# Kernel optimization log

Hardware: AMD Instinct MI355X
Metric: run time of the kernel (lower is better)

Reference implementation:

```python
import jax, jax.numpy as jnp
import numpy as np

B, S, D = 8, 4096, 768
HEADS = 12
NEIGHBORS = 2
DILATION = 1
KERNEL = 1 + 2 * NEIGHBORS  # 5
DIM_HEAD = D // HEADS


def setup_inputs() -> dict:
    key = jax.random.key(0)
    ks = jax.random.split(key, 11)
    sc = 1.0 / np.sqrt(D)
    return {
        "x": jax.random.normal(ks[0], (B, S, D), dtype=jnp.float32),
        "Wq": jax.random.normal(ks[1], (D, D), dtype=jnp.float32) * sc,
        "bq": jax.random.normal(ks[2], (D,), dtype=jnp.float32) * 0.02,
        "Wk": jax.random.normal(ks[3], (D, D), dtype=jnp.float32) * sc,
        "bk": jax.random.normal(ks[4], (D,), dtype=jnp.float32) * 0.02,
        "Wv": jax.random.normal(ks[5], (D, D), dtype=jnp.float32) * sc,
        "bv": jax.random.normal(ks[6], (D,), dtype=jnp.float32) * 0.02,
        "Wo": jax.random.normal(ks[7], (D, D), dtype=jnp.float32) * sc,
        "bo": jax.random.normal(ks[8], (D,), dtype=jnp.float32) * 0.02,
        "gamma": jnp.ones((D,), dtype=jnp.float32),
        "beta": jnp.zeros((D,), dtype=jnp.float32),
    }


def _extract_seq_patches(x, kernel_size, dilation):
    # [B, S, D] -> [B, S, kernel_size, D] of dilated local windows, zero-padded.
    seq_len = x.shape[1]
    patch_size = kernel_size + (dilation - 1) * (kernel_size - 1)
    pad_r = (patch_size - 1) // 2
    pad_l = patch_size - pad_r - 1
    xp = jnp.pad(x, ((0, 0), (pad_l, pad_r), (0, 0)))
    # small fixed loop over kernel positions (kernel_size = 5)
    return jnp.stack([xp[:, i:i + seq_len] for i in range(0, patch_size, dilation)], axis=2)


def reference(x, Wq, bq, Wk, bk, Wv, bv, Wo, bo, gamma, beta):
    patches = _extract_seq_patches(x, KERNEL, DILATION)  # [B, S, K, D]
    q = x @ Wq + bq                                       # [B, S, D]
    k = patches @ Wk + bk                                 # [B, S, K, D]
    v = patches @ Wv + bv                                 # [B, S, K, D]
    # split heads
    q = q.reshape(B, S, HEADS, DIM_HEAD)
    k = k.reshape(B, S, KERNEL, HEADS, DIM_HEAD)
    v = v.reshape(B, S, KERNEL, HEADS, DIM_HEAD)
    scale = jnp.sqrt(jnp.asarray(DIM_HEAD, dtype=q.dtype))
    scores = jnp.einsum('bshd,bskhd->bshk', q, k) / scale  # [B, S, H, K]
    p = jax.nn.softmax(scores, axis=-1)
    att = jnp.einsum('bshk,bskhd->bshd', p, v)             # [B, S, H, dh]
    att = att.reshape(B, S, D)
    att = att @ Wo + bo
    y = att + x
    # LayerNorm over last dim
    mu = jnp.mean(y, axis=-1, keepdims=True)
    var = jnp.var(y, axis=-1, keepdims=True)
    y = (y - mu) / jnp.sqrt(var + 1e-5) * gamma + beta
    return y
```

## Files before the change

kernel.cpp:

```cpp
#include <hip/hip_runtime.h>

#define B_  8
#define S_  4096
#define D_  768
#define H_  12
#define M_  (B_ * S_)
#define NQKV_ 2304
#define NTILES 12

typedef unsigned short u16;
typedef __attribute__((ext_vector_type(4))) float  f32x4;
typedef __attribute__((ext_vector_type(8))) __bf16 bf16x8;
typedef __attribute__((ext_vector_type(4))) u16    u16x4;

#define GAS __attribute__((address_space(1)))
#define LAS __attribute__((address_space(3)))

__device__ __forceinline__ u16 f2bf(float f) {
    unsigned u = __float_as_uint(f);
    u += 0x7FFF + ((u >> 16) & 1);
    return (u16)(u >> 16);
}
__device__ __forceinline__ float bf2f(u16 h) {
    return __uint_as_float(((unsigned)h) << 16);
}

__device__ __forceinline__ void gload_lds16(const void* g, void* l) {
    __builtin_amdgcn_global_load_lds((const GAS void*)g, (LAS void*)l, 16, 0, 0);
}

__device__ __forceinline__ int xcd_swz(int bid, int nwg) {
    return (bid & 7) * (nwg >> 3) + (bid >> 3);
}

__global__ __launch_bounds__(256) void castx_kernel(const float* __restrict__ x,
                                                    u16* __restrict__ xb) {
    const int i = blockIdx.x * 256 + threadIdx.x;
    const float4 v = ((const float4*)x)[i];
    u16x4 o;
    o.x = f2bf(v.x); o.y = f2bf(v.y); o.z = f2bf(v.z); o.w = f2bf(v.w);
    ((u16x4*)xb)[i] = o;
}

__global__ __launch_bounds__(256) void wtrans_kernel(const float* __restrict__ Wq,
                                                     const float* __restrict__ Wk,
                                                     const float* __restrict__ Wv,
                                                     const float* __restrict__ Wo,
                                                     u16* __restrict__ Wb) {
    const float* W = (blockIdx.z == 0) ? Wq : (blockIdx.z == 1) ? Wk
                   : (blockIdx.z == 2) ? Wv : Wo;
    u16* O = Wb + (size_t)blockIdx.z * D_ * D_;
    __shared__ float tile[32][33];
    const int tx = threadIdx.x & 31, ty = threadIdx.x >> 5;
    const int k0 = blockIdx.y * 32, n0 = blockIdx.x * 32;
#pragma unroll
    for (int j = 0; j < 4; j++)
        tile[ty + j * 8][tx] = W[(size_t)(k0 + ty + j * 8) * D_ + n0 + tx];
    __syncthreads();
#pragma unroll
    for (int j = 0; j < 4; j++)
        O[(size_t)(n0 + ty + j * 8) * D_ + k0 + tx] = f2bf(tile[tx][ty + j * 8]);
}


#define SYNC_NOVM()                                          \
    __builtin_amdgcn_sched_barrier(0);                       \
    __builtin_amdgcn_s_barrier();                            \
    asm volatile("s_waitcnt lgkmcnt(0)" ::: "memory");       \
    __builtin_amdgcn_sched_barrier(0)

#define SYNC_VM(N)                                           \
    __builtin_amdgcn_sched_barrier(0);                       \
    asm volatile("s_waitcnt vmcnt(" #N ")" ::: "memory");    \
    __builtin_amdgcn_s_barrier();                            \
    asm volatile("s_waitcnt lgkmcnt(0)" ::: "memory");       \
    __builtin_amdgcn_sched_barrier(0)

#define TRAIL()                                              \
    __builtin_amdgcn_sched_barrier(0);                       \
    __builtin_amdgcn_s_barrier()

#define MFMA_Q(AF, BF, MO, NO)                                               \
    __builtin_amdgcn_s_setprio(1);                                           \
    _Pragma("unroll") for (int mi = 0; mi < 4; ++mi)                         \
        _Pragma("unroll") for (int ni = 0; ni < 2; ++ni)                     \
            _Pragma("unroll") for (int kh = 0; kh < 2; ++kh)                 \
                acc[mi + MO][ni + NO] =                                      \
                    __builtin_amdgcn_mfma_f32_16x16x32_bf16(                 \
                        AF[mi][kh], BF[ni][kh], acc[mi + MO][ni + NO], 0, 0, 0); \
    __builtin_amdgcn_s_setprio(0)

template <int MODE>
__global__ __launch_bounds__(512, 2) void gemm8_kernel(
    const u16* __restrict__ A, const u16* __restrict__ Wb,
    const float* __restrict__ b0, const float* __restrict__ b1,
    const float* __restrict__ b2,
    u16* __restrict__ outb, const u16* __restrict__ xres) {
    extern __shared__ char lds[];

    const int t = threadIdx.x;
    const int w = t >> 6, l = t & 63;
    const int wm = w >> 2, wn = w & 3;

    const int NTN = (MODE == 0) ? 9 : 3;
    const int work = xcd_swz(blockIdx.x, gridDim.x);
    const int mt = work / NTN, nt = work % NTN;
    const int m0 = mt * 256;
    const int n0 = nt * 256;
    const int widx = (MODE == 0) ? (n0 / D_) : 3;
    const int n0w = n0 - ((MODE == 0) ? widx * D_ : 0);

    const int srow   = t >> 3;
    const int schunk = (t & 7) ^ (srow & 7);
    const u16* Asrc = A + (size_t)(m0 + srow) * D_ + schunk * 8;
    const u16* Bsrc = Wb + (size_t)widx * (D_ * D_) + (size_t)(n0w + srow) * D_ + schunk * 8;

    auto STAGE_A = [&](int h, int tk, int db) {
        const u16* s = Asrc + (size_t)(h * 128) * D_ + tk * 64;
        char* d = lds + db * 65536 + h * 16384 + (w << 10);
        gload_lds16(s, d);
        gload_lds16(s + 64 * D_, d + 8192);
    };
    auto STAGE_B = [&](int h, int tk, int db) {
        const u16* s = Bsrc + (size_t)(h * 128) * D_ + tk * 64;
        char* d = lds + db * 65536 + 32768 + h * 16384 + (w << 10);
        gload_lds16(s, d);
        gload_lds16(s + 64 * D_, d + 8192);
    };

    const int ck0 = (((l >> 4) ^ (l & 7)) << 4);
    const int ck1 = ((((l >> 4) + 4) ^ (l & 7)) << 4);
    const int aRowB = (wm * 128 + (l & 15)) * 128;
    const int bRowB = 32768 + (wn * 64 + (l & 15)) * 128;
#define LDSREAD(off) (*(const bf16x8*)(lds + (off)))

    f32x4 acc[8][4];
#pragma unroll
    for (int i = 0; i < 8; i++)
#pragma unroll
        for (int j = 0; j < 4; j++) acc[i][j] = (f32x4){0.f, 0.f, 0.f, 0.f};

    bf16x8 Alo[4][2], Ahi[4][2], Ba[2][2], Bb[2][2];

    STAGE_A(0, 0, 0); STAGE_A(1, 0, 0); STAGE_B(0, 0, 0); STAGE_B(1, 0, 0);
    STAGE_A(0, 1, 1); STAGE_A(1, 1, 1); STAGE_B(0, 1, 1);
    __builtin_amdgcn_sched_barrier(0);
    asm volatile("s_waitcnt vmcnt(6)" ::: "memory");
    __builtin_amdgcn_s_barrier();
#pragma unroll
    for (int mi = 0; mi < 4; ++mi) {
        Alo[mi][0] = LDSREAD(aRowB + mi * 2048 + ck0);
        Alo[mi][1] = LDSREAD(aRowB + mi * 2048 + ck1);
    }
#pragma unroll
    for (int ni = 0; ni < 2; ++ni) {
        Ba[ni][0] = LDSREAD(bRowB + ni * 2048 + ck0);
        Ba[ni][1] = LDSREAD(bRowB + ni * 2048 + ck1);
    }

    for (int X = 0; X < NTILES; ++X) {
        const int bX = X & 1;
        const int L0off = bX << 16;
        const int L1off = (bX ^ 1) << 16;
        int t1 = X + 1; if (t1 >= NTILES) t1 -= NTILES;
        int t2 = X + 2; if (t2 >= NTILES) t2 -= NTILES;

#pragma unroll
        for (int mi = 0; mi < 4; ++mi) {
            Ahi[mi][0] = LDSREAD(L0off + aRowB + (mi + 4) * 2048 + ck0);
            Ahi[mi][1] = LDSREAD(L0off + aRowB + (mi + 4) * 2048 + ck1);
        }
#pragma unroll
        for (int ni = 0; ni < 2; ++ni) {
            Bb[ni][0] = LDSREAD(L0off + bRowB + (ni + 2) * 2048 + ck0);
            Bb[ni][1] = LDSREAD(L0off + bRowB + (ni + 2) * 2048 + ck1);
        }
        STAGE_B(1, t1, bX ^ 1);
        SYNC_NOVM();
        MFMA_Q(Alo, Ba, 0, 0);
        TRAIL();

        STAGE_A(0, t2, bX);
        SYNC_VM(6);
        MFMA_Q(Alo, Bb, 0, 2);
        TRAIL();

#pragma unroll
        for (int mi = 0; mi < 4; ++mi) {
            Alo[mi][0] = LDSREAD(L1off + aRowB + mi * 2048 + ck0);
            Alo[mi][1] = LDSREAD(L1off + aRowB + mi * 2048 + ck1);
        }
        STAGE_A(1, t2, bX);
        SYNC_VM(4);
        MFMA_Q(Ahi, Ba, 4, 0);
        TRAIL();

#pragma unroll
        for (int ni = 0; ni < 2; ++ni) {
            Ba[ni][0] = LDSREAD(L1off + bRowB + ni * 2048 + ck0);
            Ba[ni][1] = LDSREAD(L1off + bRowB + ni * 2048 + ck1);
        }
        STAGE_B(0, t2, bX);
        SYNC_VM(6);
        MFMA_Q(Ahi, Bb, 4, 2);
        TRAIL();
    }

    const int crow0 = m0 + wm * 128 + ((l >> 4) << 2);
    const int ccol0 = n0 + wn * 64 + (l & 15);
    if (MODE == 0) {
        const float* bias = (widx == 0) ? b0 : (widx == 1) ? b1 : b2;
        const int bcol0 = ccol0 - widx * D_;
#pragma unroll
        for (int mi = 0; mi < 8; ++mi)
#pragma unroll
            for (int ni = 0; ni < 4; ++ni) {
                const float bv = bias[bcol0 + ni * 16];
#pragma unroll
                for (int r = 0; r < 4; ++r)
                    outb[(size_t)(crow0 + mi * 16 + r) * NQKV_ + ccol0 + ni * 16] =
                        f2bf(acc[mi][ni][r] + bv);
            }
    } else {
#pragma unroll
        for (int mi = 0; mi < 8; ++mi)
#pragma unroll
            for (int ni = 0; ni < 4; ++ni) {
                const int col = ccol0 + ni * 16;
                const float bv = b0[col];
#pragma unroll
                for (int r = 0; r < 4; ++r) {
                    const size_t idx = (size_t)(crow0 + mi * 16 + r) * D_ + col;
                    outb[idx] = f2bf(acc[mi][ni][r] + bv + bf2f(xres[idx]));
                }
            }
    }
}

__global__ __launch_bounds__(256) void attn_kernel(const u16* __restrict__ QKV,
                                                   const float* __restrict__ bk,
                                                   const float* __restrict__ bv,
                                                   u16* __restrict__ att) {
    const int gw = xcd_swz(blockIdx.x, gridDim.x) * 4 + (threadIdx.x >> 6);
    const int l  = threadIdx.x & 63;
    const int hq = gw % 3;
    const int m  = gw / 3;
    const int s  = m & (S_ - 1);
    const int col = hq * 256 + l * 4;
    const u16* base = QKV + (size_t)m * NQKV_;

    const u16x4 qv = *(const u16x4*)(base + col);
    float qf[4];
#pragma unroll
    for (int j = 0; j < 4; j++) qf[j] = bf2f(qv[j]);

    float sc[5];
#pragma unroll
    for (int i = 0; i < 5; i++) {
        const int sp = s + i - 2;
        float p;
        if (sp >= 0 && sp < S_) {
            const u16x4 kv = *(const u16x4*)(base + (i - 2) * NQKV_ + D_ + col);
            p = qf[0] * bf2f(kv[0]) + qf[1] * bf2f(kv[1])
              + qf[2] * bf2f(kv[2]) + qf[3] * bf2f(kv[3]);
        } else {
            const float4 kb = *(const float4*)(bk + col);
            p = qf[0] * kb.x + qf[1] * kb.y + qf[2] * kb.z + qf[3] * kb.w;
        }
#pragma unroll
        for (int off = 1; off < 16; off <<= 1) p += __shfl_xor(p, off, 64);
        sc[i] = p * 0.125f;
    }
    float mx = sc[0];
#pragma unroll
    for (int i = 1; i < 5; i++) mx = fmaxf(mx, sc[i]);
    float e[5], sum = 0.f;
#pragma unroll
    for (int i = 0; i < 5; i++) { e[i] = __expf(sc[i] - mx); sum += e[i]; }
    const float inv = 1.f / sum;

    float o[4] = {0.f, 0.f, 0.f, 0.f};
#pragma unroll
    for (int i = 0; i < 5; i++) {
        const float wgt = e[i] * inv;
        const int sp = s + i - 2;
        if (sp >= 0 && sp < S_) {
            const u16x4 vv = *(const u16x4*)(base + (i - 2) * NQKV_ + 2 * D_ + col);
#pragma unroll
            for (int j = 0; j < 4; j++) o[j] += wgt * bf2f(vv[j]);
        } else {
            const float4 vb = *(const float4*)(bv + col);
            o[0] += wgt * vb.x; o[1] += wgt * vb.y;
            o[2] += wgt * vb.z; o[3] += wgt * vb.w;
        }
    }
    u16x4 ov;
#pragma unroll
    for (int j = 0; j < 4; j++) ov[j] = f2bf(o[j]);
    *(u16x4*)(att + (size_t)m * D_ + col) = ov;
}

__global__ __launch_bounds__(256) void ln_kernel(const u16* __restrict__ Yb,
                                                 const float* __restrict__ gamma,
                                                 const float* __restrict__ beta,
                                                 float* __restrict__ out) {
    const int row = blockIdx.x;
    const u16* r = Yb + (size_t)row * D_;
    const int t = threadIdx.x;
    const float v0 = bf2f(r[t]), v1 = bf2f(r[t + 256]), v2 = bf2f(r[t + 512]);
    float s  = v0 + v1 + v2;
    float s2 = v0 * v0 + v1 * v1 + v2 * v2;
#pragma unroll
    for (int off = 32; off > 0; off >>= 1) {
        s  += __shfl_xor(s,  off, 64);
        s2 += __shfl_xor(s2, off, 64);
    }
    __shared__ float red[8];
    const int w = t >> 6, l = t & 63;
    if (l == 0) { red[w] = s; red[4 + w] = s2; }
    __syncthreads();
    s  = red[0] + red[1] + red[2] + red[3];
    s2 = red[4] + red[5] + red[6] + red[7];
    const float mu  = s * (1.f / 768.f);
    const float var = s2 * (1.f / 768.f) - mu * mu;
    const float inv = rsqrtf(var + 1e-5f);
    float* o = out + (size_t)row * D_;
    o[t]       = (v0 - mu) * inv * gamma[t]       + beta[t];
    o[t + 256] = (v1 - mu) * inv * gamma[t + 256] + beta[t + 256];
    o[t + 512] = (v2 - mu) * inv * gamma[t + 512] + beta[t + 512];
}

extern "C" void kernel_launch(void* const* d_in, const int* in_sizes, int n_in,
                              void* d_out, int out_size, void* d_ws, size_t ws_size,
                              hipStream_t stream) {
    const float* x     = (const float*)d_in[0];
    const float* Wq    = (const float*)d_in[1];
    const float* bq    = (const float*)d_in[2];
    const float* Wk    = (const float*)d_in[3];
    const float* bk    = (const float*)d_in[4];
    const float* Wv    = (const float*)d_in[5];
    const float* bv    = (const float*)d_in[6];
    const float* Wo    = (const float*)d_in[7];
    const float* bo    = (const float*)d_in[8];
    const float* gamma = (const float*)d_in[9];
    const float* beta  = (const float*)d_in[10];

    char* ws = (char*)d_ws;
    u16*   Wb  = (u16*)ws;
    u16*   xb  = (u16*)(ws + 4718592);
    u16*   QKV = (u16*)(ws + 4718592 + 50331648);
    u16*   yb  = QKV;
    u16*   att = (u16*)d_out;

    (void)hipFuncSetAttribute(reinterpret_cast<const void*>(&gemm8_kernel<0>),
                              hipFuncAttributeMaxDynamicSharedMemorySize, 131072);
    (void)hipFuncSetAttribute(reinterpret_cast<const void*>(&gemm8_kernel<1>),
                              hipFuncAttributeMaxDynamicSharedMemorySize, 131072);

    castx_kernel<<<(M_ * D_) / (256 * 4), 256, 0, stream>>>(x, xb);
    wtrans_kernel<<<dim3(24, 24, 4), 256, 0, stream>>>(Wq, Wk, Wv, Wo, Wb);
    gemm8_kernel<0><<<(M_ / 256) * 9, 512, 131072, stream>>>(xb, Wb, bq, bk, bv,
                                                             QKV, nullptr);
    attn_kernel<<<(M_ * 3) / 4, 256, 0, stream>>>(QKV, bk, bv, att);
    gemm8_kernel<1><<<(M_ / 256) * 3, 512, 131072, stream>>>(att, Wb, bo, nullptr, nullptr,
                                                             yb, xb);
    ln_kernel<<<M_, 256, 0, stream>>>(yb, gamma, beta, (float*)d_out);
}
```

Before: 354.1 us.

## Restructure GEMM main loop to one barrier per phase with reordered staging

Reworks the 8-wave GEMM pipeline so each MFMA phase ends with a single vmcnt wait plus barrier, replacing the pre-MFMA barrier, the lgkmcnt wait and the trailing barrier. The order of global-to-LDS stage issues is changed (B half first, then A halves, with adjusted vmcnt counts), and the s_setprio bracketing around MFMA blocks is removed. The goal is to cut barrier and wait overhead and let LDS reads overlap MFMAs. It risks races in buffer reuse or wrong vmcnt accounting if the new staging order does not line up with the double-buffer offsets.

```diff
diff --git a/kernel.cpp b/kernel.cpp
--- a/kernel.cpp
+++ b/kernel.cpp
@@ -63,32 +63,19 @@
 }
 
 
-#define SYNC_NOVM()                                          \
-    __builtin_amdgcn_sched_barrier(0);                       \
-    __builtin_amdgcn_s_barrier();                            \
-    asm volatile("s_waitcnt lgkmcnt(0)" ::: "memory");       \
-    __builtin_amdgcn_sched_barrier(0)
-
-#define SYNC_VM(N)                                           \
+#define PHASE_END(N)                                         \
     __builtin_amdgcn_sched_barrier(0);                       \
     asm volatile("s_waitcnt vmcnt(" #N ")" ::: "memory");    \
     __builtin_amdgcn_s_barrier();                            \
-    asm volatile("s_waitcnt lgkmcnt(0)" ::: "memory");       \
     __builtin_amdgcn_sched_barrier(0)
 
-#define TRAIL()                                              \
-    __builtin_amdgcn_sched_barrier(0);                       \
-    __builtin_amdgcn_s_barrier()
-
 #define MFMA_Q(AF, BF, MO, NO)                                               \
-    __builtin_amdgcn_s_setprio(1);                                           \
     _Pragma("unroll") for (int mi = 0; mi < 4; ++mi)                         \
         _Pragma("unroll") for (int ni = 0; ni < 2; ++ni)                     \
             _Pragma("unroll") for (int kh = 0; kh < 2; ++kh)                 \
                 acc[mi + MO][ni + NO] =                                      \
                     __builtin_amdgcn_mfma_f32_16x16x32_bf16(                 \
-                        AF[mi][kh], BF[ni][kh], acc[mi + MO][ni + NO], 0, 0, 0); \
-    __builtin_amdgcn_s_setprio(0)
+                        AF[mi][kh], BF[ni][kh], acc[mi + MO][ni + NO], 0, 0, 0)
 
 template <int MODE>
 __global__ __launch_bounds__(512, 2) void gemm8_kernel(
@@ -143,10 +130,11 @@
     bf16x8 Alo[4][2], Ahi[4][2], Ba[2][2], Bb[2][2];
 
     STAGE_A(0, 0, 0); STAGE_A(1, 0, 0); STAGE_B(0, 0, 0); STAGE_B(1, 0, 0);
-    STAGE_A(0, 1, 1); STAGE_A(1, 1, 1); STAGE_B(0, 1, 1);
+    STAGE_B(1, 1, 1); STAGE_A(0, 1, 1); STAGE_A(1, 1, 1);
     __builtin_amdgcn_sched_barrier(0);
     asm volatile("s_waitcnt vmcnt(6)" ::: "memory");
     __builtin_amdgcn_s_barrier();
+    __builtin_amdgcn_sched_barrier(0);
 #pragma unroll
     for (int mi = 0; mi < 4; ++mi) {
         Alo[mi][0] = LDSREAD(aRowB + mi * 2048 + ck0);
@@ -166,44 +154,40 @@
         int t2 = X + 2; if (t2 >= NTILES) t2 -= NTILES;
 
 #pragma unroll
+        for (int ni = 0; ni < 2; ++ni) {
+            Bb[ni][0] = LDSREAD(L0off + bRowB + (ni + 2) * 2048 + ck0);
+            Bb[ni][1] = LDSREAD(L0off + bRowB + (ni + 2) * 2048 + ck1);
+        }
+#pragma unroll
         for (int mi = 0; mi < 4; ++mi) {
             Ahi[mi][0] = LDSREAD(L0off + aRowB + (mi + 4) * 2048 + ck0);
             Ahi[mi][1] = LDSREAD(L0off + aRowB + (mi + 4) * 2048 + ck1);
         }
-#pragma unroll
-        for (int ni = 0; ni < 2; ++ni) {
-            Bb[ni][0] = LDSREAD(L0off + bRowB + (ni + 2) * 2048 + ck0);
-            Bb[ni][1] = LDSREAD(L0off + bRowB + (ni + 2) * 2048 + ck1);
-        }
-        STAGE_B(1, t1, bX ^ 1);
-        SYNC_NOVM();
+        STAGE_B(0, t1, bX ^ 1);
         MFMA_Q(Alo, Ba, 0, 0);
-        TRAIL();
-
-        STAGE_A(0, t2, bX);
-        SYNC_VM(6);
+        PHASE_END(8);
+
+        STAGE_B(1, t2, bX);
         MFMA_Q(Alo, Bb, 0, 2);
-        TRAIL();
+        PHASE_END(4);
 
 #pragma unroll
         for (int mi = 0; mi < 4; ++mi) {
             Alo[mi][0] = LDSREAD(L1off + aRowB + mi * 2048 + ck0);
             Alo[mi][1] = LDSREAD(L1off + aRowB + mi * 2048 + ck1);
         }
-        STAGE_A(1, t2, bX);
-        SYNC_VM(4);
+        STAGE_A(0, t2, bX);
         MFMA_Q(Ahi, Ba, 4, 0);
-        TRAIL();
+        PHASE_END(4);
 
 #pragma unroll
         for (int ni = 0; ni < 2; ++ni) {
             Ba[ni][0] = LDSREAD(L1off + bRowB + ni * 2048 + ck0);
             Ba[ni][1] = LDSREAD(L1off + bRowB + ni * 2048 + ck1);
         }
-        STAGE_B(0, t2, bX);
-        SYNC_VM(6);
+        STAGE_A(1, t2, bX);
         MFMA_Q(Ahi, Bb, 4, 2);
-        TRAIL();
+        PHASE_END(8);
     }
 
     const int crow0 = m0 + wm * 128 + ((l >> 4) << 2);
```

Measured after the change: 329.9 us. 6.8% less time.
